# Performance work log

Measured on AMD Instinct MI355X. Metric: run time of the kernel, lower is better.

Reference implementation:

```python
import jax, jax.numpy as jnp
import numpy as np

N_CLASS, EMB, NH = 32000, 128, 256
B, T = 2048, 256


def setup_inputs() -> dict:
    key = jax.random.key(0)
    ks = iter(jax.random.split(key, 40))
    d = {}
    d["X"] = jax.random.randint(next(ks), (B, T), 0, N_CLASS)
    d["C"] = jax.random.normal(next(ks), (N_CLASS, EMB), jnp.float32) * 0.02
    for g in "ifco":
        d[f"U_{g}1"] = jax.random.normal(next(ks), (EMB, NH), jnp.float32) / np.sqrt(EMB)
        d[f"V_{g}1"] = jax.random.normal(next(ks), (NH, NH), jnp.float32) / np.sqrt(NH)
        d[f"U_{g}2"] = jax.random.normal(next(ks), (NH, NH), jnp.float32) / np.sqrt(NH)
        d[f"V_{g}2"] = jax.random.normal(next(ks), (NH, NH), jnp.float32) / np.sqrt(NH)
        d[f"b_{g}1"] = jnp.ones((NH,), jnp.float32)
    d["W_out"] = jax.random.normal(next(ks), (NH, N_CLASS), jnp.float32) / np.sqrt(NH)
    d["b_out"] = jnp.ones((N_CLASS,), jnp.float32)
    return d


def reference(X, C,
              U_i1, V_i1, U_i2, V_i2, b_i1,
              U_f1, V_f1, U_f2, V_f2, b_f1,
              U_c1, V_c1, U_c2, V_c2, b_c1,
              U_o1, V_o1, U_o2, V_o2, b_o1,
              W_out, b_out):
    # Embed then move time to the leading axis: [T, B, EMB]
    xs = jnp.transpose(C[X], (1, 0, 2))
    Bsz = X.shape[0]
    dtype = C.dtype
    z = jnp.zeros((Bsz, NH), dtype)

    def step(carry, x):
        h1, c1, h2, c2 = carry
        # layer 1 LSTM cell
        f1 = jax.nn.sigmoid(x @ U_f1 + h1 @ V_f1 + b_f1)
        i1 = jax.nn.sigmoid(x @ U_i1 + h1 @ V_i1 + b_i1)
        g1 = jnp.tanh(x @ U_c1 + h1 @ V_c1 + b_c1)
        c1n = c1 * f1 + i1 * g1
        o1 = jax.nn.sigmoid(x @ U_o1 + h1 @ V_o1 + b_o1)
        h1n = o1 * jnp.tanh(c1n)
        # layer 2 LSTM cell (NOTE: original code reuses layer-1 biases here)
        f2 = jax.nn.sigmoid(h1n @ U_f2 + h2 @ V_f2 + b_f1)
        i2 = jax.nn.sigmoid(h1n @ U_i2 + h2 @ V_i2 + b_i1)
        g2 = jnp.tanh(h1n @ U_c2 + h2 @ V_c2 + b_c1)
        c2n = c2 * f2 + i2 * g2
        o2 = jax.nn.sigmoid(h1n @ U_o2 + h2 @ V_o2 + b_o1)
        h2n = o2 * jnp.tanh(c2n)
        return (h1n, c1n, h2n, c2n), None

    (h1, c1, h2, c2), _ = jax.lax.scan(step, (z, z, z, z), xs)
    return h2 @ W_out + b_out  # [B, N_CLASS]
```

## Files before the change

kernel.cpp:

```cpp
#include <hip/hip_runtime.h>
#include <hip/hip_bf16.h>

#define B_SZ   2048
#define T_SZ   256
#define EMB    128
#define NH     256
#define NCLASS 32000

typedef __bf16 bf16;
typedef __bf16 bf16x8 __attribute__((ext_vector_type(8)));
typedef float  f32x4  __attribute__((ext_vector_type(4)));

__device__ __forceinline__ float sigf(float x)      { return 1.0f / (1.0f + __expf(-x)); }
__device__ __forceinline__ float tanhfast(float x)  { return 2.0f / (1.0f + __expf(-2.0f * x)) - 1.0f; }

struct GatePtrs {
    const float* U1[4];
    const float* V1[4];
    const float* U2[4];
    const float* V2[4];
};

__global__ void prep_w1(GatePtrs gp, bf16* __restrict__ Wt1) {
    int gc = blockIdx.x;
    int k  = threadIdx.x;
    int g  = (gc >> 4) & 3;
    int nh = ((gc >> 6) << 4) | (gc & 15);
    float v = (k < EMB) ? gp.U1[g][k * NH + nh] : gp.V1[g][(k - EMB) * NH + nh];
    Wt1[gc * 384 + k] = (bf16)v;
}

__global__ void prep_w2(GatePtrs gp, bf16* __restrict__ Wt2) {
    int gc = blockIdx.x;
    int k  = threadIdx.x;
    int g  = (gc >> 4) & 3;
    int nh = ((gc >> 6) << 4) | (gc & 15);
    float v = (k < NH) ? gp.U2[g][k * NH + nh] : gp.V2[g][(k - NH) * NH + nh];
    Wt2[gc * 512 + k] = (bf16)v;
}

__global__ void prep_wo(const float* __restrict__ Wo, bf16* __restrict__ WoT) {
    __shared__ float tile[32][33];
    int n0 = blockIdx.x * 32;
    int k0 = blockIdx.y * 32;
    int tx = threadIdx.x & 31;
    int ty = threadIdx.x >> 5;
#pragma unroll
    for (int i = 0; i < 4; i++) {
        int k = k0 + ty + i * 8;
        tile[ty + i * 8][tx] = Wo[(size_t)k * NCLASS + n0 + tx];
    }
    __syncthreads();
#pragma unroll
    for (int i = 0; i < 4; i++) {
        int n = n0 + ty + i * 8;
        WoT[(size_t)n * NH + k0 + tx] = (bf16)tile[tx][ty + i * 8];
    }
}

__global__ __launch_bounds__(512, 1) void lstm_kernel(
    const int* __restrict__ X, const float* __restrict__ C,
    const bf16* __restrict__ Wt1, const bf16* __restrict__ Wt2,
    const float* __restrict__ bi, const float* __restrict__ bf_,
    const float* __restrict__ bc, const float* __restrict__ bo,
    bf16* __restrict__ h2out)
{
    __shared__ bf16 A1[32][392];
    __shared__ bf16 A2[32][520];

    const int tid  = threadIdx.x;
    const int lane = tid & 63;
    const int wv   = tid >> 6;
    const int cl   = lane & 15;
    const int quad = lane >> 4;
    const int gb   = blockIdx.x * 32;

    const float* bp[4] = { bi, bf_, bc, bo };
    float bias[2][4];
#pragma unroll
    for (int hg = 0; hg < 2; hg++)
#pragma unroll
        for (int g = 0; g < 4; g++)
            bias[hg][g] = bp[g][wv * 32 + hg * 16 + cl];

    for (int i = tid; i < 8192; i += 512) {
        int r = i >> 8, c = i & 255;
        A1[r][128 + c] = (bf16)0.0f;
        A2[r][256 + c] = (bf16)0.0f;
    }
    {
        int r  = tid >> 4;
        int cc = (tid & 15) * 8;
        int idx = X[(gb + r) * T_SZ + 0];
        const float* src = C + (size_t)idx * EMB + cc;
        float4 v0 = *(const float4*)(src);
        float4 v1 = *(const float4*)(src + 4);
        bf16x8 hv;
        hv[0] = (bf16)v0.x; hv[1] = (bf16)v0.y; hv[2] = (bf16)v0.z; hv[3] = (bf16)v0.w;
        hv[4] = (bf16)v1.x; hv[5] = (bf16)v1.y; hv[6] = (bf16)v1.z; hv[7] = (bf16)v1.w;
        *(bf16x8*)&A1[r][cc] = hv;
    }

    f32x4 c1s[2][2], c2s[2][2];
    const f32x4 zf = { 0.0f, 0.0f, 0.0f, 0.0f };
#pragma unroll
    for (int a = 0; a < 2; a++)
#pragma unroll
        for (int b = 0; b < 2; b++) { c1s[a][b] = zf; c2s[a][b] = zf; }

    __syncthreads();

    for (int t = 0; t < T_SZ; t++) {
        f32x4 acc[2][2][4];
#pragma unroll
        for (int mt = 0; mt < 2; mt++)
#pragma unroll
            for (int hg = 0; hg < 2; hg++)
#pragma unroll
                for (int g = 0; g < 4; g++) acc[mt][hg][g] = zf;

#pragma unroll
        for (int kt = 0; kt < 12; kt++) {
            bf16x8 a0 = *(const bf16x8*)&A1[cl][kt * 32 + quad * 8];
            bf16x8 a1 = *(const bf16x8*)&A1[16 + cl][kt * 32 + quad * 8];
#pragma unroll
            for (int hg = 0; hg < 2; hg++)
#pragma unroll
                for (int g = 0; g < 4; g++) {
                    int gc = (wv * 2 + hg) * 64 + g * 16 + cl;
                    bf16x8 b = *(const bf16x8*)(Wt1 + gc * 384 + kt * 32 + quad * 8);
                    acc[0][hg][g] = __builtin_amdgcn_mfma_f32_16x16x32_bf16(a0, b, acc[0][hg][g], 0, 0, 0);
                    acc[1][hg][g] = __builtin_amdgcn_mfma_f32_16x16x32_bf16(a1, b, acc[1][hg][g], 0, 0, 0);
                }
        }
        __syncthreads();

#pragma unroll
        for (int mt = 0; mt < 2; mt++)
#pragma unroll
            for (int hg = 0; hg < 2; hg++)
#pragma unroll
                for (int r = 0; r < 4; r++) {
                    float iv = sigf(acc[mt][hg][0][r] + bias[hg][0]);
                    float fv = sigf(acc[mt][hg][1][r] + bias[hg][1]);
                    float gv = tanhfast(acc[mt][hg][2][r] + bias[hg][2]);
                    float ov = sigf(acc[mt][hg][3][r] + bias[hg][3]);
                    float c  = c1s[mt][hg][r] * fv + iv * gv;
                    c1s[mt][hg][r] = c;
                    float h  = ov * tanhfast(c);
                    int row = mt * 16 + quad * 4 + r;
                    int col = wv * 32 + hg * 16 + cl;
                    bf16 hb = (bf16)h;
                    A1[row][128 + col] = hb;
                    A2[row][col]       = hb;
                }

        if (t + 1 < T_SZ) {
            int r  = tid >> 4;
            int cc = (tid & 15) * 8;
            int idx = X[(gb + r) * T_SZ + (t + 1)];
            const float* src = C + (size_t)idx * EMB + cc;
            float4 v0 = *(const float4*)(src);
            float4 v1 = *(const float4*)(src + 4);
            bf16x8 hv;
            hv[0] = (bf16)v0.x; hv[1] = (bf16)v0.y; hv[2] = (bf16)v0.z; hv[3] = (bf16)v0.w;
            hv[4] = (bf16)v1.x; hv[5] = (bf16)v1.y; hv[6] = (bf16)v1.z; hv[7] = (bf16)v1.w;
            *(bf16x8*)&A1[r][cc] = hv;
        }
        __syncthreads();

#pragma unroll
        for (int mt = 0; mt < 2; mt++)
#pragma unroll
            for (int hg = 0; hg < 2; hg++)
#pragma unroll
                for (int g = 0; g < 4; g++) acc[mt][hg][g] = zf;

#pragma unroll
        for (int kt = 0; kt < 16; kt++) {
            bf16x8 a0 = *(const bf16x8*)&A2[cl][kt * 32 + quad * 8];
            bf16x8 a1 = *(const bf16x8*)&A2[16 + cl][kt * 32 + quad * 8];
#pragma unroll
            for (int hg = 0; hg < 2; hg++)
#pragma unroll
                for (int g = 0; g < 4; g++) {
                    int gc = (wv * 2 + hg) * 64 + g * 16 + cl;
                    bf16x8 b = *(const bf16x8*)(Wt2 + gc * 512 + kt * 32 + quad * 8);
                    acc[0][hg][g] = __builtin_amdgcn_mfma_f32_16x16x32_bf16(a0, b, acc[0][hg][g], 0, 0, 0);
                    acc[1][hg][g] = __builtin_amdgcn_mfma_f32_16x16x32_bf16(a1, b, acc[1][hg][g], 0, 0, 0);
                }
        }
        __syncthreads();

#pragma unroll
        for (int mt = 0; mt < 2; mt++)
#pragma unroll
            for (int hg = 0; hg < 2; hg++)
#pragma unroll
                for (int r = 0; r < 4; r++) {
                    float iv = sigf(acc[mt][hg][0][r] + bias[hg][0]);
                    float fv = sigf(acc[mt][hg][1][r] + bias[hg][1]);
                    float gv = tanhfast(acc[mt][hg][2][r] + bias[hg][2]);
                    float ov = sigf(acc[mt][hg][3][r] + bias[hg][3]);
                    float c  = c2s[mt][hg][r] * fv + iv * gv;
                    c2s[mt][hg][r] = c;
                    float h  = ov * tanhfast(c);
                    int row = mt * 16 + quad * 4 + r;
                    int col = wv * 32 + hg * 16 + cl;
                    A2[row][256 + col] = (bf16)h;
                }
    }

    __syncthreads();
    for (int i = tid; i < 8192; i += 512) {
        int r = i >> 8, c = i & 255;
        h2out[(size_t)(gb + r) * NH + c] = A2[r][256 + c];
    }
}

__global__ __launch_bounds__(256, 1) void out_gemm(
    const bf16* __restrict__ h2, const bf16* __restrict__ WoT,
    const float* __restrict__ bout, float* __restrict__ out)
{
    const int tid  = threadIdx.x;
    const int lane = tid & 63;
    const int wv   = tid >> 6;
    const int cl   = lane & 15;
    const int quad = lane >> 4;
    const int nb   = blockIdx.x;
    const int mb   = blockIdx.y;
    const int mbase = mb * 64 + wv * 16;
    const int nbase = nb * 64;

    f32x4 acc[4];
    const f32x4 zf = { 0.0f, 0.0f, 0.0f, 0.0f };
#pragma unroll
    for (int nt = 0; nt < 4; nt++) acc[nt] = zf;

#pragma unroll
    for (int kt = 0; kt < 8; kt++) {
        bf16x8 a = *(const bf16x8*)(h2 + (size_t)(mbase + cl) * NH + kt * 32 + quad * 8);
#pragma unroll
        for (int nt = 0; nt < 4; nt++) {
            bf16x8 b = *(const bf16x8*)(WoT + (size_t)(nbase + nt * 16 + cl) * NH + kt * 32 + quad * 8);
            acc[nt] = __builtin_amdgcn_mfma_f32_16x16x32_bf16(a, b, acc[nt], 0, 0, 0);
        }
    }
#pragma unroll
    for (int nt = 0; nt < 4; nt++) {
        int col = nbase + nt * 16 + cl;
        float bv = bout[col];
#pragma unroll
        for (int r = 0; r < 4; r++) {
            int row = mbase + quad * 4 + r;
            out[(size_t)row * NCLASS + col] = acc[nt][r] + bv;
        }
    }
}

extern "C" void kernel_launch(void* const* d_in, const int* in_sizes, int n_in,
                              void* d_out, int out_size, void* d_ws, size_t ws_size,
                              hipStream_t stream) {
    const int*   X  = (const int*)d_in[0];
    const float* C  = (const float*)d_in[1];
    GatePtrs gp;
    for (int g = 0; g < 4; g++) {
        int base = 2 + 5 * g;
        gp.U1[g] = (const float*)d_in[base + 0];
        gp.V1[g] = (const float*)d_in[base + 1];
        gp.U2[g] = (const float*)d_in[base + 2];
        gp.V2[g] = (const float*)d_in[base + 3];
    }
    const float* bi   = (const float*)d_in[6];
    const float* bf_  = (const float*)d_in[11];
    const float* bc   = (const float*)d_in[16];
    const float* bo   = (const float*)d_in[21];
    const float* Wo   = (const float*)d_in[22];
    const float* bout = (const float*)d_in[23];
    float* out = (float*)d_out;

    char* ws = (char*)d_ws;
    bf16* Wt1 = (bf16*)(ws);
    bf16* Wt2 = (bf16*)(ws + 786432);
    bf16* WoT = (bf16*)(ws + 786432 + 1048576);
    bf16* h2w = (bf16*)(ws + 786432 + 1048576 + 16384000);

    prep_w1<<<dim3(1024), dim3(384), 0, stream>>>(gp, Wt1);
    prep_w2<<<dim3(1024), dim3(512), 0, stream>>>(gp, Wt2);
    prep_wo<<<dim3(1000, 8), dim3(256), 0, stream>>>(Wo, WoT);
    lstm_kernel<<<dim3(64), dim3(512), 0, stream>>>(X, C, Wt1, Wt2, bi, bf_, bc, bo, h2w);
    out_gemm<<<dim3(500, 32), dim3(256), 0, stream>>>(h2w, WoT, bout, out);
}
```

Before: 14.69 ms.

## Double-buffer LSTM smem, widen block to 1024 threads, pre-gather embeddings

New measurement: 13.06 ms. -11.1%, faster.

```diff
diff --git a/kernel.cpp b/kernel.cpp
--- a/kernel.cpp
+++ b/kernel.cpp
@@ -9,6 +9,7 @@
 
 typedef __bf16 bf16;
 typedef __bf16 bf16x8 __attribute__((ext_vector_type(8)));
+typedef __bf16 bf16x4 __attribute__((ext_vector_type(4)));
 typedef float  f32x4  __attribute__((ext_vector_type(4)));
 
 __device__ __forceinline__ float sigf(float x)      { return 1.0f / (1.0f + __expf(-x)); }
@@ -58,15 +59,30 @@
     }
 }
 
-__global__ __launch_bounds__(512, 1) void lstm_kernel(
+__global__ void prep_xe(const int* __restrict__ X, const float* __restrict__ C,
+                        bf16* __restrict__ Xe) {
+    size_t id = (size_t)blockIdx.x * 256 + threadIdx.x;
+    int c4 = (int)(id & 31) * 4;
+    int b  = (int)(id >> 5) & (B_SZ - 1);
+    int t  = (int)(id >> 16);
+    int idx = X[b * T_SZ + t];
+    float4 v = *(const float4*)(C + (size_t)idx * EMB + c4);
+    bf16x4 hv;
+    hv[0] = (bf16)v.x; hv[1] = (bf16)v.y; hv[2] = (bf16)v.z; hv[3] = (bf16)v.w;
+    *(bf16x4*)(Xe + ((size_t)t * B_SZ + b) * EMB + c4) = hv;
+}
+
+template<int PRE>
+__global__ __launch_bounds__(1024, 1) void lstm_kernel(
     const int* __restrict__ X, const float* __restrict__ C,
     const bf16* __restrict__ Wt1, const bf16* __restrict__ Wt2,
     const float* __restrict__ bi, const float* __restrict__ bf_,
     const float* __restrict__ bc, const float* __restrict__ bo,
+    const bf16* __restrict__ Xe,
     bf16* __restrict__ h2out)
 {
-    __shared__ bf16 A1[32][392];
-    __shared__ bf16 A2[32][520];
+    __shared__ bf16 A1[2][32][392];
+    __shared__ bf16 A2[2][32][520];
 
     const int tid  = threadIdx.x;
     const int lane = tid & 63;
@@ -76,145 +92,148 @@
     const int gb   = blockIdx.x * 32;
 
     const float* bp[4] = { bi, bf_, bc, bo };
-    float bias[2][4];
-#pragma unroll
-    for (int hg = 0; hg < 2; hg++)
-#pragma unroll
-        for (int g = 0; g < 4; g++)
-            bias[hg][g] = bp[g][wv * 32 + hg * 16 + cl];
-
-    for (int i = tid; i < 8192; i += 512) {
+    float bias[4];
+#pragma unroll
+    for (int g = 0; g < 4; g++) bias[g] = bp[g][wv * 16 + cl];
+
+    const bf16* w1p[4];
+    const bf16* w2p[4];
+#pragma unroll
+    for (int g = 0; g < 4; g++) {
+        int gc = wv * 64 + g * 16 + cl;
+        w1p[g] = Wt1 + gc * 384 + quad * 8;
+        w2p[g] = Wt2 + gc * 512 + quad * 8;
+    }
+
+    for (int i = tid; i < 8192; i += 1024) {
         int r = i >> 8, c = i & 255;
-        A1[r][128 + c] = (bf16)0.0f;
-        A2[r][256 + c] = (bf16)0.0f;
+        A1[0][r][128 + c] = (bf16)0.0f;
+        A2[0][r][256 + c] = (bf16)0.0f;
     }
     {
-        int r  = tid >> 4;
-        int cc = (tid & 15) * 8;
-        int idx = X[(gb + r) * T_SZ + 0];
-        const float* src = C + (size_t)idx * EMB + cc;
-        float4 v0 = *(const float4*)(src);
-        float4 v1 = *(const float4*)(src + 4);
-        bf16x8 hv;
-        hv[0] = (bf16)v0.x; hv[1] = (bf16)v0.y; hv[2] = (bf16)v0.z; hv[3] = (bf16)v0.w;
-        hv[4] = (bf16)v1.x; hv[5] = (bf16)v1.y; hv[6] = (bf16)v1.z; hv[7] = (bf16)v1.w;
-        *(bf16x8*)&A1[r][cc] = hv;
-    }
-
-    f32x4 c1s[2][2], c2s[2][2];
+        int r  = tid >> 5;
+        int cc = (tid & 31) * 4;
+        if (PRE) {
+            bf16x4 hv = *(const bf16x4*)(Xe + ((size_t)0 * B_SZ + gb + r) * EMB + cc);
+            *(bf16x4*)&A1[0][r][cc] = hv;
+        } else {
+            int idx = X[(gb + r) * T_SZ + 0];
+            float4 v = *(const float4*)(C + (size_t)idx * EMB + cc);
+            bf16x4 hv;
+            hv[0] = (bf16)v.x; hv[1] = (bf16)v.y; hv[2] = (bf16)v.z; hv[3] = (bf16)v.w;
+            *(bf16x4*)&A1[0][r][cc] = hv;
+        }
+    }
+
+    f32x4 c1s[2], c2s[2];
     const f32x4 zf = { 0.0f, 0.0f, 0.0f, 0.0f };
 #pragma unroll
-    for (int a = 0; a < 2; a++)
-#pragma unroll
-        for (int b = 0; b < 2; b++) { c1s[a][b] = zf; c2s[a][b] = zf; }
+    for (int mt = 0; mt < 2; mt++) { c1s[mt] = zf; c2s[mt] = zf; }
 
     __syncthreads();
 
     for (int t = 0; t < T_SZ; t++) {
-        f32x4 acc[2][2][4];
+        const int p = t & 1;
+
+        f32x4 acc[2][4];
 #pragma unroll
         for (int mt = 0; mt < 2; mt++)
 #pragma unroll
-            for (int hg = 0; hg < 2; hg++)
-#pragma unroll
-                for (int g = 0; g < 4; g++) acc[mt][hg][g] = zf;
-
-#pragma unroll
-        for (int kt = 0; kt < 12; kt++) {
-            bf16x8 a0 = *(const bf16x8*)&A1[cl][kt * 32 + quad * 8];
-            bf16x8 a1 = *(const bf16x8*)&A1[16 + cl][kt * 32 + quad * 8];
-#pragma unroll
-            for (int hg = 0; hg < 2; hg++)
+            for (int g = 0; g < 4; g++) acc[mt][g] = zf;
+
+        {
+            const bf16* a0p = &A1[p][cl][quad * 8];
+            const bf16* a1p = &A1[p][16 + cl][quad * 8];
+#pragma unroll
+            for (int kt = 0; kt < 12; kt++) {
+                bf16x8 a0 = *(const bf16x8*)(a0p + kt * 32);
+                bf16x8 a1 = *(const bf16x8*)(a1p + kt * 32);
 #pragma unroll
                 for (int g = 0; g < 4; g++) {
-                    int gc = (wv * 2 + hg) * 64 + g * 16 + cl;
-                    bf16x8 b = *(const bf16x8*)(Wt1 + gc * 384 + kt * 32 + quad * 8);
-                    acc[0][hg][g] = __builtin_amdgcn_mfma_f32_16x16x32_bf16(a0, b, acc[0][hg][g], 0, 0, 0);
-                    acc[1][hg][g] = __builtin_amdgcn_mfma_f32_16x16x32_bf16(a1, b, acc[1][hg][g], 0, 0, 0);
+                    bf16x8 b = *(const bf16x8*)(w1p[g] + kt * 32);
+                    acc[0][g] = __builtin_amdgcn_mfma_f32_16x16x32_bf16(a0, b, acc[0][g], 0, 0, 0);
+                    acc[1][g] = __builtin_amdgcn_mfma_f32_16x16x32_bf16(a1, b, acc[1][g], 0, 0, 0);
                 }
-        }
+            }
+        }
+
+#pragma unroll
+        for (int mt = 0; mt < 2; mt++)
+#pragma unroll
+            for (int r = 0; r < 4; r++) {
+                float iv = sigf(acc[mt][0][r] + bias[0]);
+                float fv = sigf(acc[mt][1][r] + bias[1]);
+                float gv = tanhfast(acc[mt][2][r] + bias[2]);
+                float ov = sigf(acc[mt][3][r] + bias[3]);
+                float c  = c1s[mt][r] * fv + iv * gv;
+                c1s[mt][r] = c;
+                float h  = ov * tanhfast(c);
+                int row = mt * 16 + quad * 4 + r;
+                int col = wv * 16 + cl;
+                bf16 hb = (bf16)h;
+                A1[p ^ 1][row][128 + col] = hb;
+                A2[p][row][col]           = hb;
+            }
+
+        if (t + 1 < T_SZ) {
+            int r  = tid >> 5;
+            int cc = (tid & 31) * 4;
+            if (PRE) {
+                bf16x4 hv = *(const bf16x4*)(Xe + ((size_t)(t + 1) * B_SZ + gb + r) * EMB + cc);
+                *(bf16x4*)&A1[p ^ 1][r][cc] = hv;
+            } else {
+                int idx = X[(gb + r) * T_SZ + (t + 1)];
+                float4 v = *(const float4*)(C + (size_t)idx * EMB + cc);
+                bf16x4 hv;
+                hv[0] = (bf16)v.x; hv[1] = (bf16)v.y; hv[2] = (bf16)v.z; hv[3] = (bf16)v.w;
+                *(bf16x4*)&A1[p ^ 1][r][cc] = hv;
+            }
+        }
+
         __syncthreads();
 
 #pragma unroll
         for (int mt = 0; mt < 2; mt++)
 #pragma unroll
-            for (int hg = 0; hg < 2; hg++)
-#pragma unroll
-                for (int r = 0; r < 4; r++) {
-                    float iv = sigf(acc[mt][hg][0][r] + bias[hg][0]);
-                    float fv = sigf(acc[mt][hg][1][r] + bias[hg][1]);
-                    float gv = tanhfast(acc[mt][hg][2][r] + bias[hg][2]);
-                    float ov = sigf(acc[mt][hg][3][r] + bias[hg][3]);
-                    float c  = c1s[mt][hg][r] * fv + iv * gv;
-                    c1s[mt][hg][r] = c;
-                    float h  = ov * tanhfast(c);
-                    int row = mt * 16 + quad * 4 + r;
-                    int col = wv * 32 + hg * 16 + cl;
-                    bf16 hb = (bf16)h;
-                    A1[row][128 + col] = hb;
-                    A2[row][col]       = hb;
+            for (int g = 0; g < 4; g++) acc[mt][g] = zf;
+
+        {
+            const bf16* a0p = &A2[p][cl][quad * 8];
+            const bf16* a1p = &A2[p][16 + cl][quad * 8];
+#pragma unroll
+            for (int kt = 0; kt < 16; kt++) {
+                bf16x8 a0 = *(const bf16x8*)(a0p + kt * 32);
+                bf16x8 a1 = *(const bf16x8*)(a1p + kt * 32);
+#pragma unroll
+                for (int g = 0; g < 4; g++) {
+                    bf16x8 b = *(const bf16x8*)(w2p[g] + kt * 32);
+                    acc[0][g] = __builtin_amdgcn_mfma_f32_16x16x32_bf16(a0, b, acc[0][g], 0, 0, 0);
+                    acc[1][g] = __builtin_amdgcn_mfma_f32_16x16x32_bf16(a1, b, acc[1][g], 0, 0, 0);
                 }
-
-        if (t + 1 < T_SZ) {
-            int r  = tid >> 4;
-            int cc = (tid & 15) * 8;
-            int idx = X[(gb + r) * T_SZ + (t + 1)];
-            const float* src = C + (size_t)idx * EMB + cc;
-            float4 v0 = *(const float4*)(src);
-            float4 v1 = *(const float4*)(src + 4);
-            bf16x8 hv;
-            hv[0] = (bf16)v0.x; hv[1] = (bf16)v0.y; hv[2] = (bf16)v0.z; hv[3] = (bf16)v0.w;
-            hv[4] = (bf16)v1.x; hv[5] = (bf16)v1.y; hv[6] = (bf16)v1.z; hv[7] = (bf16)v1.w;
-            *(bf16x8*)&A1[r][cc] = hv;
-        }
-        __syncthreads();
+            }
+        }
 
 #pragma unroll
         for (int mt = 0; mt < 2; mt++)
 #pragma unroll
-            for (int hg = 0; hg < 2; hg++)
-#pragma unroll
-                for (int g = 0; g < 4; g++) acc[mt][hg][g] = zf;
-
-#pragma unroll
-        for (int kt = 0; kt < 16; kt++) {
-            bf16x8 a0 = *(const bf16x8*)&A2[cl][kt * 32 + quad * 8];
-            bf16x8 a1 = *(const bf16x8*)&A2[16 + cl][kt * 32 + quad * 8];
-#pragma unroll
-            for (int hg = 0; hg < 2; hg++)
-#pragma unroll
-                for (int g = 0; g < 4; g++) {
-                    int gc = (wv * 2 + hg) * 64 + g * 16 + cl;
-                    bf16x8 b = *(const bf16x8*)(Wt2 + gc * 512 + kt * 32 + quad * 8);
-                    acc[0][hg][g] = __builtin_amdgcn_mfma_f32_16x16x32_bf16(a0, b, acc[0][hg][g], 0, 0, 0);
-                    acc[1][hg][g] = __builtin_amdgcn_mfma_f32_16x16x32_bf16(a1, b, acc[1][hg][g], 0, 0, 0);
-                }
-        }
-        __syncthreads();
-
-#pragma unroll
-        for (int mt = 0; mt < 2; mt++)
-#pragma unroll
-            for (int hg = 0; hg < 2; hg++)
-#pragma unroll
-                for (int r = 0; r < 4; r++) {
-                    float iv = sigf(acc[mt][hg][0][r] + bias[hg][0]);
-                    float fv = sigf(acc[mt][hg][1][r] + bias[hg][1]);
-                    float gv = tanhfast(acc[mt][hg][2][r] + bias[hg][2]);
-                    float ov = sigf(acc[mt][hg][3][r] + bias[hg][3]);
-                    float c  = c2s[mt][hg][r] * fv + iv * gv;
-                    c2s[mt][hg][r] = c;
-                    float h  = ov * tanhfast(c);
-                    int row = mt * 16 + quad * 4 + r;
-                    int col = wv * 32 + hg * 16 + cl;
-                    A2[row][256 + col] = (bf16)h;
-                }
+            for (int r = 0; r < 4; r++) {
+                float iv = sigf(acc[mt][0][r] + bias[0]);
+                float fv = sigf(acc[mt][1][r] + bias[1]);
+                float gv = tanhfast(acc[mt][2][r] + bias[2]);
+                float ov = sigf(acc[mt][3][r] + bias[3]);
+                float c  = c2s[mt][r] * fv + iv * gv;
+                c2s[mt][r] = c;
+                float h  = ov * tanhfast(c);
+                int row = mt * 16 + quad * 4 + r;
+                int col = wv * 16 + cl;
+                A2[p ^ 1][row][256 + col] = (bf16)h;
+            }
     }
 
     __syncthreads();
-    for (int i = tid; i < 8192; i += 512) {
+    for (int i = tid; i < 8192; i += 1024) {
         int r = i >> 8, c = i & 255;
-        h2out[(size_t)(gb + r) * NH + c] = A2[r][256 + c];
+        h2out[(size_t)(gb + r) * NH + c] = A2[0][r][256 + c];
     }
 }
 
@@ -284,10 +303,19 @@
     bf16* Wt2 = (bf16*)(ws + 786432);
     bf16* WoT = (bf16*)(ws + 786432 + 1048576);
     bf16* h2w = (bf16*)(ws + 786432 + 1048576 + 16384000);
+    bf16* Xe  = (bf16*)(ws + 786432 + 1048576 + 16384000 + 1048576);
+    const size_t WS_NEED_XE = 786432ull + 1048576 + 16384000 + 1048576 + 134217728;
 
     prep_w1<<<dim3(1024), dim3(384), 0, stream>>>(gp, Wt1);
     prep_w2<<<dim3(1024), dim3(512), 0, stream>>>(gp, Wt2);
     prep_wo<<<dim3(1000, 8), dim3(256), 0, stream>>>(Wo, WoT);
-    lstm_kernel<<<dim3(64), dim3(512), 0, stream>>>(X, C, Wt1, Wt2, bi, bf_, bc, bo, h2w);
+
+    if (ws_size >= WS_NEED_XE) {
+        prep_xe<<<dim3(65536), dim3(256), 0, stream>>>(X, C, Xe);
+        lstm_kernel<1><<<dim3(64), dim3(1024), 0, stream>>>(X, C, Wt1, Wt2, bi, bf_, bc, bo, Xe, h2w);
+    } else {
+        lstm_kernel<0><<<dim3(64), dim3(1024), 0, stream>>>(X, C, Wt1, Wt2, bi, bf_, bc, bo, Xe, h2w);
+    }
+
     out_gemm<<<dim3(500, 32), dim3(256), 0, stream>>>(h2w, WoT, bout, out);
 }
```
